# Optimization experiments

Hardware: AMD Instinct MI355X
Metric: run time of the kernel (lower is better)

The kernel has to match this reference:

```python
import jax, jax.numpy as jnp
import numpy as np

N = 50000; E = 400000; H = 8; D = 32; CD = 768; SD = 128; OUT = 2; HD = H * D


def gat_conv(x, src, dst, W, a_src, a_dst, b):
    """PyG-style GATConv (concat heads, self-loops, LeakyReLU 0.2, eval mode)."""
    n = x.shape[0]
    loops = jnp.arange(n, dtype=src.dtype)
    s = jnp.concatenate([src, loops])
    t = jnp.concatenate([dst, loops])
    h = (x @ W).reshape(n, H, D)                      # [N,H,D]
    a_s = (h * a_src).sum(-1)                          # [N,H]
    a_d = (h * a_dst).sum(-1)                          # [N,H]
    e = jax.nn.leaky_relu(a_s[s] + a_d[t], 0.2)        # [E+N,H]
    m = jax.ops.segment_max(e, t, num_segments=n)
    m = jnp.where(jnp.isfinite(m), m, 0.0)
    ex = jnp.exp(e - m[t])
    den = jax.ops.segment_sum(ex, t, num_segments=n)
    alpha = ex / (den[t] + 1e-16)                      # segment softmax over incoming edges
    out = jax.ops.segment_sum(alpha[:, :, None] * h[s], t, num_segments=n)
    return out.reshape(n, HD) + b


def setup_inputs():
    key = jax.random.key(0)
    ks = jax.random.split(key, 32)
    inp = {}
    inp['content_x'] = jax.random.normal(ks[0], (N, CD), jnp.float32)
    inp['social_x'] = jax.random.normal(ks[1], (N, SD), jnp.float32)
    inp['content_edge_index'] = jax.random.randint(ks[2], (2, E), 0, N, dtype=jnp.int32)
    inp['social_edge_index'] = jax.random.randint(ks[3], (2, E), 0, N, dtype=jnp.int32)
    i = 4
    def mk(shape, scale=0.05):
        nonlocal i
        w = jax.random.normal(ks[i], shape, jnp.float32) * scale
        i += 1
        return w
    # content GAT layers
    inp['Wc0'] = mk((CD, HD)); inp['ac0s'] = mk((H, D)); inp['ac0d'] = mk((H, D)); inp['bc0'] = jnp.zeros((HD,), jnp.float32)
    inp['Wc1'] = mk((HD, HD)); inp['ac1s'] = mk((H, D)); inp['ac1d'] = mk((H, D)); inp['bc1'] = jnp.zeros((HD,), jnp.float32)
    # social GAT layers
    inp['Ws0'] = mk((SD, HD)); inp['as0s'] = mk((H, D)); inp['as0d'] = mk((H, D)); inp['bs0'] = jnp.zeros((HD,), jnp.float32)
    inp['Ws1'] = mk((HD, HD)); inp['as1s'] = mk((H, D)); inp['as1d'] = mk((H, D)); inp['bs1'] = jnp.zeros((HD,), jnp.float32)
    # dual channel attention (Linear(HD,1) each)
    inp['attc_w'] = mk((HD, 1)); inp['attc_b'] = jnp.zeros((1,), jnp.float32)
    inp['atts_w'] = mk((HD, 1)); inp['atts_b'] = jnp.zeros((1,), jnp.float32)
    # MLP head
    inp['fc1_w'] = mk((2 * HD, D)); inp['fc1_b'] = jnp.zeros((D,), jnp.float32)
    inp['fc2_w'] = mk((D, OUT)); inp['fc2_b'] = jnp.zeros((OUT,), jnp.float32)
    return inp


def reference(content_x, social_x, content_edge_index, social_edge_index,
              Wc0, ac0s, ac0d, bc0, Wc1, ac1s, ac1d, bc1,
              Ws0, as0s, as0d, bs0, Ws1, as1s, as1d, bs1,
              attc_w, attc_b, atts_w, atts_b,
              fc1_w, fc1_b, fc2_w, fc2_b):
    cs, cd = content_edge_index[0], content_edge_index[1]
    ss, sd = social_edge_index[0], social_edge_index[1]
    c = jax.nn.elu(gat_conv(content_x, cs, cd, Wc0, ac0s, ac0d, bc0))
    c = jax.nn.elu(gat_conv(c, cs, cd, Wc1, ac1s, ac1d, bc1))
    s = jax.nn.elu(gat_conv(social_x, ss, sd, Ws0, as0s, as0d, bs0))
    s = jax.nn.elu(gat_conv(s, ss, sd, Ws1, as1s, as1d, bs1))
    c_score = jax.nn.sigmoid(c @ attc_w + attc_b)      # [N,1]
    s_score = jax.nn.sigmoid(s @ atts_w + atts_b)      # [N,1]
    w = jax.nn.softmax(jnp.concatenate([c_score, s_score], axis=1), axis=1)  # [N,2]
    x = jnp.concatenate([c * w[:, 0:1], s * w[:, 1:2]], axis=1)
    x = jax.nn.elu(x @ fc1_w + fc1_b)
    x = x @ fc2_w + fc2_b
    return jax.nn.log_softmax(x, axis=1)
```

## Files before the change

### kernel.cpp

```cpp
#include <hip/hip_runtime.h>
#include <cstddef>
#include <cstdint>

#define HD 256
#define NHEAD 8
#define CAP 64

typedef __attribute__((ext_vector_type(8))) short bf16x8;
typedef __attribute__((ext_vector_type(4))) float f32x4;

__device__ __forceinline__ unsigned short f2bf(float f) {
    unsigned u = __float_as_uint(f);
    u += 0x7fffu + ((u >> 16) & 1u);
    return (unsigned short)(u >> 16);
}
__device__ __forceinline__ float bf2f(unsigned short h) {
    return __uint_as_float(((unsigned)h) << 16);
}

__device__ __forceinline__ void gload16(const unsigned short* g, unsigned short* l) {
    __builtin_amdgcn_global_load_lds((const __attribute__((address_space(1))) unsigned int*)g,
                                     (__attribute__((address_space(3))) unsigned int*)l,
                                     16, 0, 0);
}

__global__ __launch_bounds__(256) void zero32_k(int* __restrict__ p, int n) {
    int i = blockIdx.x * 256 + threadIdx.x;
    if (i < n) p[i] = 0;
}

__global__ __launch_bounds__(256) void bucket_fill_k(const int* __restrict__ src,
                                                     const int* __restrict__ dst,
                                                     int* __restrict__ cnt,
                                                     int* __restrict__ bkt, int E) {
    int e = blockIdx.x * 256 + threadIdx.x;
    if (e >= E) return;
    int t = dst[e];
    int pos = atomicAdd(&cnt[t], 1);
    if (pos < CAP) bkt[(size_t)t * CAP + pos] = src[e];
}

__global__ __launch_bounds__(256) void split_k(const float* __restrict__ x,
                                               unsigned short* __restrict__ hi,
                                               unsigned short* __restrict__ lo,
                                               int n4) {
    int i = blockIdx.x * 256 + threadIdx.x;
    int stride = gridDim.x * 256;
    for (; i < n4; i += stride) {
        float4 v = ((const float4*)x)[i];
        ushort4 h, l;
        h.x = f2bf(v.x); l.x = f2bf(v.x - bf2f(h.x));
        h.y = f2bf(v.y); l.y = f2bf(v.y - bf2f(h.y));
        h.z = f2bf(v.z); l.z = f2bf(v.z - bf2f(h.z));
        h.w = f2bf(v.w); l.w = f2bf(v.w - bf2f(h.w));
        ((ushort4*)hi)[i] = h;
        ((ushort4*)lo)[i] = l;
    }
}

__global__ __launch_bounds__(256) void wsplit_k(const float* __restrict__ W,
                                                unsigned short* __restrict__ hi,
                                                unsigned short* __restrict__ lo, int K) {
    int idx = blockIdx.x * 256 + threadIdx.x;
    if (idx >= K * HD) return;
    int n = idx / K, k = idx - n * K;
    float v = W[(size_t)k * HD + n];
    unsigned short h = f2bf(v);
    hi[idx] = h;
    lo[idx] = f2bf(v - bf2f(h));
}

__global__ __launch_bounds__(256, 2) void gemm_mfma_k(
    const unsigned short* __restrict__ Ahi, const unsigned short* __restrict__ Alo,
    const unsigned short* __restrict__ Bhi, const unsigned short* __restrict__ Blo,
    float* __restrict__ C, int M, int K) {
    __shared__ unsigned short smem[4 * 128 * 32];
    const int tid = threadIdx.x;
    const int lane = tid & 63;
    const int wv = tid >> 6;
    const int Rw = (wv >> 1) * 64;
    const int Cw = (wv & 1) * 64;
    const int bm = blockIdx.y * 128;
    const int bn = blockIdx.x * 128;

    const int sr0 = tid >> 2;
    const int p = tid & 3;
    const int g0 = p ^ ((sr0 >> 1) & 3);
    const int g1 = p ^ (((sr0 + 64) >> 1) & 3);
    int ar0 = bm + sr0;      if (ar0 >= M) ar0 = M - 1;
    int ar1 = bm + sr0 + 64; if (ar1 >= M) ar1 = M - 1;
    const int bc0 = bn + sr0;
    const int bc1 = bn + sr0 + 64;
    const size_t aoff0 = (size_t)ar0 * K + g0 * 8;
    const size_t aoff1 = (size_t)ar1 * K + g1 * 8;
    const size_t boff0 = (size_t)bc0 * K + g0 * 8;
    const size_t boff1 = (size_t)bc1 * K + g1 * 8;

    unsigned short* sAh = smem;
    unsigned short* sAl = smem + 4096;
    unsigned short* sBh = smem + 8192;
    unsigned short* sBl = smem + 12288;
    const int ldsb = wv * 512;

    f32x4 acc[4][4];
#pragma unroll
    for (int m = 0; m < 4; m++)
#pragma unroll
        for (int n = 0; n < 4; n++) acc[m][n] = (f32x4){0.f, 0.f, 0.f, 0.f};

    const int r16 = lane & 15, gq = lane >> 4;
    const int rsw = gq ^ ((r16 >> 1) & 3);

    for (int k0 = 0; k0 < K; k0 += 32) {
        __syncthreads();
        gload16(Ahi + aoff0 + k0, sAh + ldsb);
        gload16(Ahi + aoff1 + k0, sAh + 2048 + ldsb);
        gload16(Alo + aoff0 + k0, sAl + ldsb);
        gload16(Alo + aoff1 + k0, sAl + 2048 + ldsb);
        gload16(Bhi + boff0 + k0, sBh + ldsb);
        gload16(Bhi + boff1 + k0, sBh + 2048 + ldsb);
        gload16(Blo + boff0 + k0, sBl + ldsb);
        gload16(Blo + boff1 + k0, sBl + 2048 + ldsb);
        __syncthreads();

        bf16x8 ah[4], al[4], bh[4], bl[4];
#pragma unroll
        for (int m = 0; m < 4; m++) {
            int off = (Rw + m * 16 + r16) * 32 + rsw * 8;
            ah[m] = *(const bf16x8*)(sAh + off);
            al[m] = *(const bf16x8*)(sAl + off);
        }
#pragma unroll
        for (int n = 0; n < 4; n++) {
            int off = (Cw + n * 16 + r16) * 32 + rsw * 8;
            bh[n] = *(const bf16x8*)(sBh + off);
            bl[n] = *(const bf16x8*)(sBl + off);
        }
#pragma unroll
        for (int m = 0; m < 4; m++)
#pragma unroll
            for (int n = 0; n < 4; n++) {
                acc[m][n] = __builtin_amdgcn_mfma_f32_16x16x32_bf16(ah[m], bh[n], acc[m][n], 0, 0, 0);
                acc[m][n] = __builtin_amdgcn_mfma_f32_16x16x32_bf16(ah[m], bl[n], acc[m][n], 0, 0, 0);
                acc[m][n] = __builtin_amdgcn_mfma_f32_16x16x32_bf16(al[m], bh[n], acc[m][n], 0, 0, 0);
            }
    }

#pragma unroll
    for (int m = 0; m < 4; m++) {
        int rbase = bm + Rw + m * 16 + ((lane >> 4) << 2);
#pragma unroll
        for (int n = 0; n < 4; n++) {
            int col = bn + Cw + n * 16 + r16;
            float* cp = C + (size_t)rbase * HD + col;
            f32x4 v = acc[m][n];
#pragma unroll
            for (int r = 0; r < 4; r++)
                if (rbase + r < M) cp[(size_t)r * HD] = v[r];
        }
    }
}

__global__ __launch_bounds__(256) void attscore_k(const float* __restrict__ h,
                                                  const float* __restrict__ a_src,
                                                  const float* __restrict__ a_dst,
                                                  float* __restrict__ out_s,
                                                  float* __restrict__ out_d, int n) {
    int idx = blockIdx.x * 256 + threadIdx.x;
    if (idx >= n * NHEAD) return;
    int head = idx & 7;
    const float* hp = h + (size_t)(idx >> 3) * HD + head * 32;
    const float* ap = a_src + head * 32;
    const float* dp = a_dst + head * 32;
    float s = 0.f, d = 0.f;
#pragma unroll
    for (int j = 0; j < 32; j += 4) {
        float4 hv = *(const float4*)(hp + j);
        float4 av = *(const float4*)(ap + j);
        float4 dv = *(const float4*)(dp + j);
        s += hv.x * av.x + hv.y * av.y + hv.z * av.z + hv.w * av.w;
        d += hv.x * dv.x + hv.y * dv.y + hv.z * dv.z + hv.w * dv.w;
    }
    out_s[idx] = s;
    out_d[idx] = d;
}

__device__ __forceinline__ float leaky02(float x) { return x > 0.f ? x : 0.2f * x; }

__global__ __launch_bounds__(256) void agg_k(const float* __restrict__ h,
                                             const float* __restrict__ a_s,
                                             const float* __restrict__ a_d,
                                             const int* __restrict__ cnt,
                                             const int* __restrict__ bkt,
                                             const float* __restrict__ bias,
                                             float* __restrict__ out,
                                             unsigned short* __restrict__ ohi,
                                             unsigned short* __restrict__ olo, int n) {
    int wid = (blockIdx.x * 256 + threadIdx.x) >> 6;
    if (wid >= n) return;
    int lane = threadIdx.x & 63;
    int head = lane >> 3;
    const float4* h4 = (const float4*)h;

    float adt = a_d[wid * NHEAD + head];
    float m = leaky02(a_s[wid * NHEAD + head] + adt);
    float den = 1.f;
    float4 hv = h4[(size_t)wid * 64 + lane];
    float ax = hv.x, ay = hv.y, az = hv.z, aw = hv.w;

    int k = cnt[wid]; if (k > CAP) k = CAP;
    const int* bp = bkt + (size_t)wid * CAP;
    for (int i = 0; i < k; i++) {
        int s = bp[i];
        float e = leaky02(a_s[s * NHEAD + head] + adt);
        float nm = fmaxf(m, e);
        float corr = __expf(m - nm);
        float pp = __expf(e - nm);
        float4 v = h4[(size_t)s * 64 + lane];
        den = den * corr + pp;
        ax = ax * corr + pp * v.x;
        ay = ay * corr + pp * v.y;
        az = az * corr + pp * v.z;
        aw = aw * corr + pp * v.w;
        m = nm;
    }
    float inv = 1.f / den;
    float4 bv = *(const float4*)(bias + lane * 4);
    float ox = fmaf(ax, inv, bv.x);
    float oy = fmaf(ay, inv, bv.y);
    float oz = fmaf(az, inv, bv.z);
    float ow = fmaf(aw, inv, bv.w);
    ox = ox > 0.f ? ox : expm1f(ox);
    oy = oy > 0.f ? oy : expm1f(oy);
    oz = oz > 0.f ? oz : expm1f(oz);
    ow = ow > 0.f ? ow : expm1f(ow);
    ((float4*)out)[(size_t)wid * 64 + lane] = make_float4(ox, oy, oz, ow);
    if (ohi) {
        ushort4 h4o, l4o;
        h4o.x = f2bf(ox); l4o.x = f2bf(ox - bf2f(h4o.x));
        h4o.y = f2bf(oy); l4o.y = f2bf(oy - bf2f(h4o.y));
        h4o.z = f2bf(oz); l4o.z = f2bf(oz - bf2f(h4o.z));
        h4o.w = f2bf(ow); l4o.w = f2bf(ow - bf2f(h4o.w));
        ((ushort4*)ohi)[(size_t)wid * 64 + lane] = h4o;
        ((ushort4*)olo)[(size_t)wid * 64 + lane] = l4o;
    }
}

__global__ __launch_bounds__(256) void head_k(const float* __restrict__ cb,
                                              const float* __restrict__ sb,
                                              const float* __restrict__ attc_w,
                                              const float* __restrict__ attc_b,
                                              const float* __restrict__ atts_w,
                                              const float* __restrict__ atts_b,
                                              const float* __restrict__ fc1_w,
                                              const float* __restrict__ fc1_b,
                                              const float* __restrict__ fc2_w,
                                              const float* __restrict__ fc2_b,
                                              float* __restrict__ out, int n) {
    int wid = (blockIdx.x * 256 + threadIdx.x) >> 6;
    if (wid >= n) return;
    int lane = threadIdx.x & 63;
    const float* c = cb + (size_t)wid * HD;
    const float* s = sb + (size_t)wid * HD;

    float4 cv = *(const float4*)(c + lane * 4);
    float4 wc = *(const float4*)(attc_w + lane * 4);
    float4 sv = *(const float4*)(s + lane * 4);
    float4 ws = *(const float4*)(atts_w + lane * 4);
    float pc = cv.x * wc.x + cv.y * wc.y + cv.z * wc.z + cv.w * wc.w;
    float ps = sv.x * ws.x + sv.y * ws.y + sv.z * ws.z + sv.w * ws.w;
#pragma unroll
    for (int o = 32; o; o >>= 1) { pc += __shfl_xor(pc, o); ps += __shfl_xor(ps, o); }
    float csc = 1.f / (1.f + __expf(-(pc + attc_b[0])));
    float ssc = 1.f / (1.f + __expf(-(ps + atts_b[0])));
    float mx0 = fmaxf(csc, ssc);
    float e0 = __expf(csc - mx0), e1 = __expf(ssc - mx0);
    float w0 = e0 / (e0 + e1), w1 = e1 / (e0 + e1);

    int col = lane & 31, half = lane >> 5;
    const float* xb = half ? s : c;
    float wsc = half ? w1 : w0;
    const float* fw = fc1_w + (size_t)half * HD * 32 + col;
    float acc = 0.f;
#pragma unroll 4
    for (int kk = 0; kk < HD; kk++) acc = fmaf(xb[kk], fw[kk * 32], acc);
    acc *= wsc;
    float y = acc + __shfl_xor(acc, 32) + fc1_b[col];
    y = y > 0.f ? y : expm1f(y);
    float v = y * fc2_w[col * 2 + half];
#pragma unroll
    for (int o = 16; o; o >>= 1) v += __shfl_xor(v, o);
    float z0 = __shfl(v, 0), z1 = __shfl(v, 32);
    if (lane == 0) {
        float zm = fmaxf(z0, z1);
        float lse = zm + log1pf(__expf(fminf(z0, z1) - zm));
        out[(size_t)wid * 2]     = z0 - lse;
        out[(size_t)wid * 2 + 1] = z1 - lse;
    }
}

extern "C" void kernel_launch(void* const* d_in, const int* in_sizes, int n_in,
                              void* d_out, int out_size, void* d_ws, size_t ws_size,
                              hipStream_t stream) {
    (void)n_in; (void)out_size; (void)ws_size;
    const float* content_x = (const float*)d_in[0];
    const float* social_x  = (const float*)d_in[1];
    const int*   cei = (const int*)d_in[2];
    const int*   sei = (const int*)d_in[3];
    const float* Wc0  = (const float*)d_in[4];
    const float* ac0s = (const float*)d_in[5];
    const float* ac0d = (const float*)d_in[6];
    const float* bc0  = (const float*)d_in[7];
    const float* Wc1  = (const float*)d_in[8];
    const float* ac1s = (const float*)d_in[9];
    const float* ac1d = (const float*)d_in[10];
    const float* bc1  = (const float*)d_in[11];
    const float* Ws0  = (const float*)d_in[12];
    const float* as0s = (const float*)d_in[13];
    const float* as0d = (const float*)d_in[14];
    const float* bs0  = (const float*)d_in[15];
    const float* Ws1  = (const float*)d_in[16];
    const float* as1s = (const float*)d_in[17];
    const float* as1d = (const float*)d_in[18];
    const float* bs1  = (const float*)d_in[19];
    const float* attc_w = (const float*)d_in[20];
    const float* attc_b = (const float*)d_in[21];
    const float* atts_w = (const float*)d_in[22];
    const float* atts_b = (const float*)d_in[23];
    const float* fc1_w  = (const float*)d_in[24];
    const float* fc1_b  = (const float*)d_in[25];
    const float* fc2_w  = (const float*)d_in[26];
    const float* fc2_b  = (const float*)d_in[27];

    const int E  = in_sizes[2] / 2;
    const int CD = in_sizes[4] / HD;
    const int SD = in_sizes[12] / HD;
    const int n  = in_sizes[0] / CD;

    char* p = (char*)d_ws;
    auto carve = [&](size_t bytes) { char* q = p; p += (bytes + 255) & ~(size_t)255; return q; };
    float* hbuf = (float*)carve((size_t)n * HD * 4);
    float* cbuf = (float*)carve((size_t)n * HD * 4);
    float* sbuf = (float*)carve((size_t)n * HD * 4);
    unsigned short* Xhi = (unsigned short*)carve((size_t)n * CD * 2);
    unsigned short* Xlo = (unsigned short*)carve((size_t)n * CD * 2);
    float* asb  = (float*)carve((size_t)n * NHEAD * 4);
    float* adb  = (float*)carve((size_t)n * NHEAD * 4);
    int* cnt_c  = (int*)carve((size_t)n * 4);
    int* cnt_s  = (int*)carve((size_t)n * 4);
    int* bkt_c  = (int*)carve((size_t)n * CAP * 4);
    int* bkt_s  = (int*)carve((size_t)n * CAP * 4);
    unsigned short* Wc0h = (unsigned short*)carve((size_t)CD * HD * 2);
    unsigned short* Wc0l = (unsigned short*)carve((size_t)CD * HD * 2);
    unsigned short* Wc1h = (unsigned short*)carve((size_t)HD * HD * 2);
    unsigned short* Wc1l = (unsigned short*)carve((size_t)HD * HD * 2);
    unsigned short* Ws0h = (unsigned short*)carve((size_t)SD * HD * 2);
    unsigned short* Ws0l = (unsigned short*)carve((size_t)SD * HD * 2);
    unsigned short* Ws1h = (unsigned short*)carve((size_t)HD * HD * 2);
    unsigned short* Ws1l = (unsigned short*)carve((size_t)HD * HD * 2);

    dim3 b256(256);
    zero32_k<<<dim3((n + 255) / 256), b256, 0, stream>>>(cnt_c, n);
    zero32_k<<<dim3((n + 255) / 256), b256, 0, stream>>>(cnt_s, n);
    bucket_fill_k<<<dim3((E + 255) / 256), b256, 0, stream>>>(cei, cei + E, cnt_c, bkt_c, E);
    bucket_fill_k<<<dim3((E + 255) / 256), b256, 0, stream>>>(sei, sei + E, cnt_s, bkt_s, E);

    wsplit_k<<<dim3((CD * HD + 255) / 256), b256, 0, stream>>>(Wc0, Wc0h, Wc0l, CD);
    wsplit_k<<<dim3((HD * HD + 255) / 256), b256, 0, stream>>>(Wc1, Wc1h, Wc1l, HD);
    wsplit_k<<<dim3((SD * HD + 255) / 256), b256, 0, stream>>>(Ws0, Ws0h, Ws0l, SD);
    wsplit_k<<<dim3((HD * HD + 255) / 256), b256, 0, stream>>>(Ws1, Ws1h, Ws1l, HD);

    dim3 gg(2, (n + 127) / 128);
    dim3 nb8((n * NHEAD + 255) / 256);
    dim3 nwave((n + 3) / 4);

    split_k<<<dim3(2048), b256, 0, stream>>>(content_x, Xhi, Xlo, n * CD / 4);
    gemm_mfma_k<<<gg, b256, 0, stream>>>(Xhi, Xlo, Wc0h, Wc0l, hbuf, n, CD);
    attscore_k<<<nb8, b256, 0, stream>>>(hbuf, ac0s, ac0d, asb, adb, n);
    agg_k<<<nwave, b256, 0, stream>>>(hbuf, asb, adb, cnt_c, bkt_c, bc0, cbuf, Xhi, Xlo, n);
    gemm_mfma_k<<<gg, b256, 0, stream>>>(Xhi, Xlo, Wc1h, Wc1l, hbuf, n, HD);
    attscore_k<<<nb8, b256, 0, stream>>>(hbuf, ac1s, ac1d, asb, adb, n);
    agg_k<<<nwave, b256, 0, stream>>>(hbuf, asb, adb, cnt_c, bkt_c, bc1, cbuf,
                                      (unsigned short*)nullptr, (unsigned short*)nullptr, n);
    split_k<<<dim3(2048), b256, 0, stream>>>(social_x, Xhi, Xlo, n * SD / 4);
    gemm_mfma_k<<<gg, b256, 0, stream>>>(Xhi, Xlo, Ws0h, Ws0l, hbuf, n, SD);
    attscore_k<<<nb8, b256, 0, stream>>>(hbuf, as0s, as0d, asb, adb, n);
    agg_k<<<nwave, b256, 0, stream>>>(hbuf, asb, adb, cnt_s, bkt_s, bs0, sbuf, Xhi, Xlo, n);
    gemm_mfma_k<<<gg, b256, 0, stream>>>(Xhi, Xlo, Ws1h, Ws1l, hbuf, n, HD);
    attscore_k<<<nb8, b256, 0, stream>>>(hbuf, as1s, as1d, asb, adb, n);
    agg_k<<<nwave, b256, 0, stream>>>(hbuf, asb, adb, cnt_s, bkt_s, bs1, sbuf,
                                      (unsigned short*)nullptr, (unsigned short*)nullptr, n);

    head_k<<<nwave, b256, 0, stream>>>(cbuf, sbuf, attc_w, attc_b, atts_w, atts_b,
                                       fc1_w, fc1_b, fc2_w, fc2_b, (float*)d_out, n);
}
```

Before: 1.152 ms.

## Overlap neighbor gathers in aggregation and stage fc1 weights in LDS for head

The aggregation kernel loads the neighbor index list once per wave and broadcasts each index with shuffles. It keeps four independent online-softmax accumulators so four neighbor gathers can be in flight at once, then merges them at the end. The head kernel stages fc1 weights in shared memory, processes 64 nodes per block, and splits the dot product into 8 partial sums to raise ILP. This costs more registers and a 64KB LDS tile per head block, which may lower occupancy.

Measured after the change: 1.123 ms. 2.5% less time.

```diff
diff --git a/kernel.cpp b/kernel.cpp
--- a/kernel.cpp
+++ b/kernel.cpp
@@ -203,27 +203,72 @@
     const float4* h4 = (const float4*)h;
 
     float adt = a_d[wid * NHEAD + head];
-    float m = leaky02(a_s[wid * NHEAD + head] + adt);
-    float den = 1.f;
-    float4 hv = h4[(size_t)wid * 64 + lane];
-    float ax = hv.x, ay = hv.y, az = hv.z, aw = hv.w;
-
     int k = cnt[wid]; if (k > CAP) k = CAP;
     const int* bp = bkt + (size_t)wid * CAP;
-    for (int i = 0; i < k; i++) {
-        int s = bp[i];
+    int sj = bp[lane];
+
+    float m0 = leaky02(a_s[wid * NHEAD + head] + adt), den0 = 1.f;
+    float4 hv = h4[(size_t)wid * 64 + lane];
+    float4 A0 = hv, A1 = {0,0,0,0}, A2 = {0,0,0,0}, A3 = {0,0,0,0};
+    float m1 = -3.0e38f, m2 = -3.0e38f, m3 = -3.0e38f;
+    float den1 = 0.f, den2 = 0.f, den3 = 0.f;
+
+    int i = 0;
+    for (; i + 3 < k; i += 4) {
+        int s0 = __shfl(sj, i), s1 = __shfl(sj, i + 1);
+        int s2 = __shfl(sj, i + 2), s3 = __shfl(sj, i + 3);
+        float e0 = a_s[s0 * NHEAD + head];
+        float e1 = a_s[s1 * NHEAD + head];
+        float e2 = a_s[s2 * NHEAD + head];
+        float e3 = a_s[s3 * NHEAD + head];
+        float4 v0 = h4[(size_t)s0 * 64 + lane];
+        float4 v1 = h4[(size_t)s1 * 64 + lane];
+        float4 v2 = h4[(size_t)s2 * 64 + lane];
+        float4 v3 = h4[(size_t)s3 * 64 + lane];
+        e0 = leaky02(e0 + adt); e1 = leaky02(e1 + adt);
+        e2 = leaky02(e2 + adt); e3 = leaky02(e3 + adt);
+        {
+            float nm = fmaxf(m0, e0), c = __expf(m0 - nm), pp = __expf(e0 - nm);
+            den0 = den0 * c + pp;
+            A0.x = A0.x * c + pp * v0.x; A0.y = A0.y * c + pp * v0.y;
+            A0.z = A0.z * c + pp * v0.z; A0.w = A0.w * c + pp * v0.w; m0 = nm;
+        }
+        {
+            float nm = fmaxf(m1, e1), c = __expf(m1 - nm), pp = __expf(e1 - nm);
+            den1 = den1 * c + pp;
+            A1.x = A1.x * c + pp * v1.x; A1.y = A1.y * c + pp * v1.y;
+            A1.z = A1.z * c + pp * v1.z; A1.w = A1.w * c + pp * v1.w; m1 = nm;
+        }
+        {
+            float nm = fmaxf(m2, e2), c = __expf(m2 - nm), pp = __expf(e2 - nm);
+            den2 = den2 * c + pp;
+            A2.x = A2.x * c + pp * v2.x; A2.y = A2.y * c + pp * v2.y;
+            A2.z = A2.z * c + pp * v2.z; A2.w = A2.w * c + pp * v2.w; m2 = nm;
+        }
+        {
+            float nm = fmaxf(m3, e3), c = __expf(m3 - nm), pp = __expf(e3 - nm);
+            den3 = den3 * c + pp;
+            A3.x = A3.x * c + pp * v3.x; A3.y = A3.y * c + pp * v3.y;
+            A3.z = A3.z * c + pp * v3.z; A3.w = A3.w * c + pp * v3.w; m3 = nm;
+        }
+    }
+    for (; i < k; i++) {
+        int s = __shfl(sj, i);
         float e = leaky02(a_s[s * NHEAD + head] + adt);
-        float nm = fmaxf(m, e);
-        float corr = __expf(m - nm);
-        float pp = __expf(e - nm);
         float4 v = h4[(size_t)s * 64 + lane];
-        den = den * corr + pp;
-        ax = ax * corr + pp * v.x;
-        ay = ay * corr + pp * v.y;
-        az = az * corr + pp * v.z;
-        aw = aw * corr + pp * v.w;
-        m = nm;
-    }
+        float nm = fmaxf(m0, e), c = __expf(m0 - nm), pp = __expf(e - nm);
+        den0 = den0 * c + pp;
+        A0.x = A0.x * c + pp * v.x; A0.y = A0.y * c + pp * v.y;
+        A0.z = A0.z * c + pp * v.z; A0.w = A0.w * c + pp * v.w; m0 = nm;
+    }
+    float M = fmaxf(fmaxf(m0, m1), fmaxf(m2, m3));
+    float c0 = __expf(m0 - M), c1 = __expf(m1 - M), c2 = __expf(m2 - M), c3 = __expf(m3 - M);
+    float den = den0 * c0 + den1 * c1 + den2 * c2 + den3 * c3;
+    float ax = A0.x * c0 + A1.x * c1 + A2.x * c2 + A3.x * c3;
+    float ay = A0.y * c0 + A1.y * c1 + A2.y * c2 + A3.y * c3;
+    float az = A0.z * c0 + A1.z * c1 + A2.z * c2 + A3.z * c3;
+    float aw = A0.w * c0 + A1.w * c1 + A2.w * c2 + A3.w * c3;
+
     float inv = 1.f / den;
     float4 bv = *(const float4*)(bias + lane * 4);
     float ox = fmaf(ax, inv, bv.x);
@@ -257,45 +302,70 @@
                                               const float* __restrict__ fc2_w,
                                               const float* __restrict__ fc2_b,
                                               float* __restrict__ out, int n) {
-    int wid = (blockIdx.x * 256 + threadIdx.x) >> 6;
-    if (wid >= n) return;
-    int lane = threadIdx.x & 63;
-    const float* c = cb + (size_t)wid * HD;
-    const float* s = sb + (size_t)wid * HD;
-
-    float4 cv = *(const float4*)(c + lane * 4);
+    __shared__ float w1s[512 * 32];
+    const int tid = threadIdx.x;
+    for (int j = tid; j < 512 * 32 / 4; j += 256)
+        ((float4*)w1s)[j] = ((const float4*)fc1_w)[j];
+    __syncthreads();
+
+    const int lane = tid & 63;
+    const int wv = tid >> 6;
+    const int col = lane & 31, half = lane >> 5;
+    const float f2w = fc2_w[col * 2 + half];
+    const float f1b = fc1_b[col];
+    const float b20 = fc2_b[0], b21 = fc2_b[1];
+    const float acb = attc_b[0], asb_ = atts_b[0];
     float4 wc = *(const float4*)(attc_w + lane * 4);
-    float4 sv = *(const float4*)(s + lane * 4);
     float4 ws = *(const float4*)(atts_w + lane * 4);
-    float pc = cv.x * wc.x + cv.y * wc.y + cv.z * wc.z + cv.w * wc.w;
-    float ps = sv.x * ws.x + sv.y * ws.y + sv.z * ws.z + sv.w * ws.w;
-#pragma unroll
-    for (int o = 32; o; o >>= 1) { pc += __shfl_xor(pc, o); ps += __shfl_xor(ps, o); }
-    float csc = 1.f / (1.f + __expf(-(pc + attc_b[0])));
-    float ssc = 1.f / (1.f + __expf(-(ps + atts_b[0])));
-    float mx0 = fmaxf(csc, ssc);
-    float e0 = __expf(csc - mx0), e1 = __expf(ssc - mx0);
-    float w0 = e0 / (e0 + e1), w1 = e1 / (e0 + e1);
-
-    int col = lane & 31, half = lane >> 5;
-    const float* xb = half ? s : c;
-    float wsc = half ? w1 : w0;
-    const float* fw = fc1_w + (size_t)half * HD * 32 + col;
-    float acc = 0.f;
+    const float* wp = w1s + (size_t)half * 256 * 32 + col;
+
+    for (int it = 0; it < 16; it++) {
+        int nd = blockIdx.x * 64 + wv * 16 + it;
+        if (nd >= n) break;
+        const float* c = cb + (size_t)nd * HD;
+        const float* s = sb + (size_t)nd * HD;
+        float4 cv = ((const float4*)c)[lane];
+        float4 sv = ((const float4*)s)[lane];
+        float pc = cv.x * wc.x + cv.y * wc.y + cv.z * wc.z + cv.w * wc.w;
+        float ps = sv.x * ws.x + sv.y * ws.y + sv.z * ws.z + sv.w * ws.w;
+#pragma unroll
+        for (int o = 32; o; o >>= 1) { pc += __shfl_xor(pc, o); ps += __shfl_xor(ps, o); }
+        float csc = 1.f / (1.f + __expf(-(pc + acb)));
+        float ssc = 1.f / (1.f + __expf(-(ps + asb_)));
+        float mx0 = fmaxf(csc, ssc);
+        float e0 = __expf(csc - mx0), e1 = __expf(ssc - mx0);
+        float w0 = e0 / (e0 + e1), w1 = e1 / (e0 + e1);
+
+        const float4* xb4 = (const float4*)(half ? s : c);
+        float wsc = half ? w1 : w0;
+        float a0 = 0.f, a1 = 0.f, a2 = 0.f, a3 = 0.f, a4 = 0.f, a5 = 0.f, a6 = 0.f, a7 = 0.f;
 #pragma unroll 4
-    for (int kk = 0; kk < HD; kk++) acc = fmaf(xb[kk], fw[kk * 32], acc);
-    acc *= wsc;
-    float y = acc + __shfl_xor(acc, 32) + fc1_b[col];
-    y = y > 0.f ? y : expm1f(y);
-    float v = y * fc2_w[col * 2 + half];
-#pragma unroll
-    for (int o = 16; o; o >>= 1) v += __shfl_xor(v, o);
-    float z0 = __shfl(v, 0), z1 = __shfl(v, 32);
-    if (lane == 0) {
-        float zm = fmaxf(z0, z1);
-        float lse = zm + log1pf(__expf(fminf(z0, z1) - zm));
-        out[(size_t)wid * 2]     = z0 - lse;
-        out[(size_t)wid * 2 + 1] = z1 - lse;
+        for (int kk = 0; kk < 256; kk += 8) {
+            float4 x0 = xb4[kk >> 2];
+            float4 x1 = xb4[(kk >> 2) + 1];
+            a0 = fmaf(x0.x, wp[(kk + 0) * 32], a0);
+            a1 = fmaf(x0.y, wp[(kk + 1) * 32], a1);
+            a2 = fmaf(x0.z, wp[(kk + 2) * 32], a2);
+            a3 = fmaf(x0.w, wp[(kk + 3) * 32], a3);
+            a4 = fmaf(x1.x, wp[(kk + 4) * 32], a4);
+            a5 = fmaf(x1.y, wp[(kk + 5) * 32], a5);
+            a6 = fmaf(x1.z, wp[(kk + 6) * 32], a6);
+            a7 = fmaf(x1.w, wp[(kk + 7) * 32], a7);
+        }
+        float acc = ((a0 + a1) + (a2 + a3)) + ((a4 + a5) + (a6 + a7));
+        acc *= wsc;
+        float y = acc + __shfl_xor(acc, 32) + f1b;
+        y = y > 0.f ? y : expm1f(y);
+        float v = y * f2w;
+#pragma unroll
+        for (int o = 16; o; o >>= 1) v += __shfl_xor(v, o);
+        float z0 = __shfl(v, 0) + b20, z1 = __shfl(v, 32) + b21;
+        if (lane == 0) {
+            float zm = fmaxf(z0, z1);
+            float lse = zm + log1pf(__expf(fminf(z0, z1) - zm));
+            out[(size_t)nd * 2]     = z0 - lse;
+            out[(size_t)nd * 2 + 1] = z1 - lse;
+        }
     }
 }
 
@@ -391,6 +461,6 @@
     agg_k<<<nwave, b256, 0, stream>>>(hbuf, asb, adb, cnt_s, bkt_s, bs1, sbuf,
                                       (unsigned short*)nullptr, (unsigned short*)nullptr, n);
 
-    head_k<<<nwave, b256, 0, stream>>>(cbuf, sbuf, attc_w, attc_b, atts_w, atts_b,
-                                       fc1_w, fc1_b, fc2_w, fc2_b, (float*)d_out, n);
-}
+    head_k<<<dim3((n + 63) / 64), b256, 0, stream>>>(cbuf, sbuf, attc_w, attc_b, atts_w, atts_b,
+                                                     fc1_w, fc1_b, fc2_w, fc2_b, (float*)d_out, n);
+}
```
